# Kernel optimization log

Hardware: AMD Instinct MI355X
Metric: run time of the kernel (lower is better)

The kernel has to match this reference:

```python
import jax, jax.numpy as jnp
import numpy as np

B, N_INST, C, K, H, W = 4, 64, 16, 4, 480, 480


def setup_inputs() -> dict:
    key = jax.random.key(0)
    k1, k2 = jax.random.split(key)
    # one binary-ish channel per instance, values in [0,1]
    update_map = jax.random.uniform(k1, (B, N_INST, H, W), dtype=jnp.float32)
    # current global instance-ID map, one channel per semantic category
    init_instance_map = jax.random.randint(k2, (B, C, H, W), 0, 50).astype(jnp.int32)
    # instance channel indices grouped by category (category c owns K instances)
    instance_ids = jnp.broadcast_to(
        jnp.arange(C * K, dtype=jnp.int32).reshape(C, K), (B, C, K)
    )
    return {
        "update_map": update_map,
        "init_instance_map": init_instance_map,
        "instance_ids": instance_ids,
    }


def reference(update_map, init_instance_map, instance_ids):
    b, n_inst, h, w = update_map.shape
    _, c, k = instance_ids.shape
    L = n_inst + 1  # local IDs live in [0, n_inst]
    BIG = jnp.int32(2 ** 30)

    # ---- aggregate instance channels per category (one-hot collapse) ----
    # gather the K instance channels of each category: [B, C, K, H, W]
    oh = jnp.take_along_axis(
        update_map[:, None, :, :, :],
        instance_ids[:, :, :, None, None].astype(jnp.int32),
        axis=2,
    )
    bg = jnp.full((b, c, 1, h, w), 1e-5, update_map.dtype)  # background plane
    idx = jnp.argmax(jnp.concatenate([bg, oh], axis=2), axis=2)  # [B, C, H, W]
    # remap argmax index -> instance ID via [0] + instance_ids
    padded_ids = jnp.concatenate(
        [jnp.zeros((b, c, 1), jnp.int32), instance_ids.astype(jnp.int32)], axis=2
    )  # [B, C, K+1]
    agg = padded_ids[
        jnp.arange(b)[:, None, None, None],
        jnp.arange(c)[None, :, None, None],
        idx,
    ]  # [B, C, H, W] local instance-ID map per category

    # ---- merge local IDs into global map, per env, sequential over categories ----
    def merge_env(gmap0, agg_e):
        def step(gmap, ci):
            local = agg_e[ci].reshape(-1)
            glob = gmap[ci].reshape(-1)
            max_id = jnp.max(gmap)  # max over ALL categories so far (sequential dep)
            # smallest overlapping nonzero global ID per local ID (torch.unique()[0])
            overlap_min = jax.ops.segment_min(
                jnp.where(glob != 0, glob, BIG), local, num_segments=L
            )
            present = jax.ops.segment_sum(
                jnp.ones_like(local), local, num_segments=L
            ) > 0
            has_overlap = overlap_min < BIG
            is_new = (present & (~has_overlap)).at[0].set(False)
            new_id = max_id + jnp.cumsum(is_new.astype(jnp.int32))
            mapping = jnp.where(has_overlap, overlap_min, jnp.where(is_new, new_id, 0))
            mapping = mapping.at[0].set(0)
            new_glob = jnp.maximum(glob, mapping[local]).reshape(h, w)
            updated = jnp.where(jnp.sum(agg_e[ci]) > 0, new_glob, gmap[ci])
            return gmap.at[ci].set(updated), None

        gmap, _ = jax.lax.scan(step, gmap0, jnp.arange(c))
        return gmap

    return jax.vmap(merge_env)(init_instance_map, agg)
```

## Files before the change

kernel.cpp:

```cpp
#include <hip/hip_runtime.h>
#include <stdint.h>
#include <limits.h>

#define BB 4
#define NI 64
#define CC 16
#define KK 4
#define HH 480
#define WW 480
#define PLANE (HH * WW)
#define NG (PLANE / 4)
#define BPP 45
#define GPT 5
#define TPB 256
#define BIGV (1 << 30)
#define NPLANE (BB * CC)

typedef float  v4f __attribute__((ext_vector_type(4)));
typedef int    v4i __attribute__((ext_vector_type(4)));

#define SEL8_BYTES ((size_t)NPLANE * PLANE)
#define PART_STRIDE 8
#define MAP_OFF (NPLANE * BPP * PART_STRIDE)

__device__ __forceinline__ int wred_min(int v) {
    for (int o = 32; o; o >>= 1) v = min(v, __shfl_down(v, o, 64));
    return v;
}
__device__ __forceinline__ int wred_max(int v) {
    for (int o = 32; o; o >>= 1) v = max(v, __shfl_down(v, o, 64));
    return v;
}
__device__ __forceinline__ int wred_or(int v) {
    for (int o = 32; o; o >>= 1) v |= __shfl_down(v, o, 64);
    return v;
}

__global__ __launch_bounds__(TPB) void stats_kernel(
    const float* __restrict__ update, const int* __restrict__ initmap,
    const int* __restrict__ inst_ids, unsigned int* __restrict__ sel8,
    int* __restrict__ wsi) {
    int plane = blockIdx.x / BPP;
    int chunk = blockIdx.x % BPP;
    int b = plane >> 4;

    int idbase = plane * KK;
    int id0 = inst_ids[idbase + 0], id1 = inst_ids[idbase + 1];
    int id2 = inst_ids[idbase + 2], id3 = inst_ids[idbase + 3];

    const v4f* u0 = (const v4f*)(update + ((size_t)b * NI + id0) * PLANE);
    const v4f* u1 = (const v4f*)(update + ((size_t)b * NI + id1) * PLANE);
    const v4f* u2 = (const v4f*)(update + ((size_t)b * NI + id2) * PLANE);
    const v4f* u3 = (const v4f*)(update + ((size_t)b * NI + id3) * PLANE);
    const v4i* gl = (const v4i*)(initmap + (size_t)plane * PLANE);
    unsigned int* sp = sel8 + (size_t)plane * NG;

    int lmin0 = INT_MAX, lmin1 = INT_MAX, lmin2 = INT_MAX, lmin3 = INT_MAX;
    int pres = 0, gmax = 0;

    int base = chunk * (TPB * GPT);
#pragma unroll
    for (int it = 0; it < GPT; it++) {
        int g = base + it * TPB + threadIdx.x;
        v4f a  = __builtin_nontemporal_load(&u0[g]);
        v4f b2 = __builtin_nontemporal_load(&u1[g]);
        v4f c  = __builtin_nontemporal_load(&u2[g]);
        v4f d  = __builtin_nontemporal_load(&u3[g]);
        v4i gv = __builtin_nontemporal_load(&gl[g]);

        unsigned int packed = 0;
#pragma unroll
        for (int e = 0; e < 4; e++) {
            float best = 1e-5f; int s = 0;
            if (a[e]  > best) { best = a[e];  s = 1; }
            if (b2[e] > best) { best = b2[e]; s = 2; }
            if (c[e]  > best) { best = c[e];  s = 3; }
            if (d[e]  > best) { s = 4; }
            int gve = gv[e];
            packed |= (unsigned int)(s * 50 + gve) << (8 * e);
            gmax = max(gmax, gve);
            if (s) {
                int kk = s - 1; pres |= 1 << kk;
                int v = gve ? gve : BIGV;
                if (kk == 0) lmin0 = min(lmin0, v);
                else if (kk == 1) lmin1 = min(lmin1, v);
                else if (kk == 2) lmin2 = min(lmin2, v);
                else lmin3 = min(lmin3, v);
            }
        }
        sp[g] = packed;
    }

    lmin0 = wred_min(lmin0); lmin1 = wred_min(lmin1);
    lmin2 = wred_min(lmin2); lmin3 = wred_min(lmin3);
    pres = wred_or(pres); gmax = wred_max(gmax);

    __shared__ int red[4][6];
    int wv = threadIdx.x >> 6, lane = threadIdx.x & 63;
    if (lane == 0) {
        red[wv][0] = lmin0; red[wv][1] = lmin1; red[wv][2] = lmin2;
        red[wv][3] = lmin3; red[wv][4] = pres;  red[wv][5] = gmax;
    }
    __syncthreads();
    if (threadIdx.x == 0) {
        int m0 = red[0][0], m1 = red[0][1], m2 = red[0][2], m3 = red[0][3];
        int pr = red[0][4], gm = red[0][5];
        for (int w2 = 1; w2 < 4; w2++) {
            m0 = min(m0, red[w2][0]); m1 = min(m1, red[w2][1]);
            m2 = min(m2, red[w2][2]); m3 = min(m3, red[w2][3]);
            pr |= red[w2][4]; gm = max(gm, red[w2][5]);
        }
        int* pp = wsi + ((size_t)plane * BPP + chunk) * PART_STRIDE;
        pp[0] = m0; pp[1] = m1; pp[2] = m2; pp[3] = m3; pp[4] = pr; pp[5] = gm;
    }
}

__global__ void mapping_kernel(const int* __restrict__ inst_ids, int* wsi) {
    __shared__ int s_ov[NPLANE][4];
    __shared__ int s_pr[NPLANE];
    __shared__ int s_gm[NPLANE];

    int plane = threadIdx.x;
    int m0 = INT_MAX, m1 = INT_MAX, m2 = INT_MAX, m3 = INT_MAX, pr = 0, gm = 0;
    for (int ch = 0; ch < BPP; ch++) {
        const int* pp = wsi + ((size_t)plane * BPP + ch) * PART_STRIDE;
        m0 = min(m0, pp[0]); m1 = min(m1, pp[1]);
        m2 = min(m2, pp[2]); m3 = min(m3, pp[3]);
        pr |= pp[4]; gm = max(gm, pp[5]);
    }
    s_ov[plane][0] = m0; s_ov[plane][1] = m1;
    s_ov[plane][2] = m2; s_ov[plane][3] = m3;
    s_pr[plane] = pr; s_gm[plane] = gm;
    __syncthreads();

    if (threadIdx.x < BB) {
        int b = threadIdx.x;
        int max_id = 0;
        for (int ci = 0; ci < CC; ci++) max_id = max(max_id, s_gm[b * CC + ci]);
        for (int ci = 0; ci < CC; ci++) {
            int pl = b * CC + ci;
            int base = pl * KK;
            int id[KK], ov[KK], prb[KK];
            int prbits = s_pr[pl];
            for (int t = 0; t < KK; t++) {
                id[t] = inst_ids[base + t];
                ov[t] = s_ov[pl][t];
                prb[t] = (prbits >> t) & 1;
            }
            int ord[KK] = {0, 1, 2, 3};
            for (int i = 1; i < KK; i++) {
                int key = ord[i], j = i - 1;
                while (j >= 0 && id[ord[j]] > id[key]) { ord[j + 1] = ord[j]; j--; }
                ord[j + 1] = key;
            }
            int map_slot[KK];
            int prev_id = -1, cur_map = 0, cnt_new = 0;
            for (int j = 0; j < KK; j++) {
                int s = ord[j], l = id[s];
                if (l != prev_id) {
                    int cov = INT_MAX, cpr = 0;
                    for (int t = 0; t < KK; t++)
                        if (id[t] == l) { cov = min(cov, ov[t]); cpr |= prb[t]; }
                    if (l == 0) cur_map = 0;
                    else {
                        bool has = cov < BIGV;
                        bool isnew = cpr && !has;
                        if (isnew) { cnt_new++; cur_map = max_id + cnt_new; }
                        else cur_map = has ? cov : 0;
                    }
                    prev_id = l;
                }
                map_slot[s] = cur_map;
            }
            for (int t = 0; t < KK; t++) wsi[MAP_OFF + base + t] = map_slot[t];
            max_id += cnt_new;
        }
    }
}

__global__ __launch_bounds__(TPB) void remap_kernel(
    const unsigned int* __restrict__ sel8, const int* __restrict__ wsi,
    int* __restrict__ out) {
    int plane = blockIdx.x / BPP;
    int chunk = blockIdx.x % BPP;

    int m0 = wsi[MAP_OFF + plane * 4 + 0];
    int m1 = wsi[MAP_OFF + plane * 4 + 1];
    int m2 = wsi[MAP_OFF + plane * 4 + 2];
    int m3 = wsi[MAP_OFF + plane * 4 + 3];

    const unsigned int* sp = sel8 + (size_t)plane * NG;
    v4i* op = (v4i*)(out + (size_t)plane * PLANE);

    int base = chunk * (TPB * GPT);
#pragma unroll
    for (int it = 0; it < GPT; it++) {
        int g = base + it * TPB + threadIdx.x;
        unsigned int u = sp[g];
        v4i ov;
#pragma unroll
        for (int e = 0; e < 4; e++) {
            unsigned int p = (u >> (8 * e)) & 0xFFu;
            int s = (int)((p * 41u) >> 11);
            int gvv = (int)p - s * 50;
            int mv = (s == 1) ? m0 : (s == 2) ? m1 : (s == 3) ? m2 : m3;
            ov[e] = s ? max(gvv, mv) : gvv;
        }
        __builtin_nontemporal_store(ov, &op[g]);
    }
}

extern "C" void kernel_launch(void* const* d_in, const int* in_sizes, int n_in,
                              void* d_out, int out_size, void* d_ws, size_t ws_size,
                              hipStream_t stream) {
    const float* update = (const float*)d_in[0];
    const int* initmap = (const int*)d_in[1];
    const int* inst_ids = (const int*)d_in[2];
    int* out = (int*)d_out;

    unsigned int* sel8 = (unsigned int*)d_ws;
    int* wsi = (int*)((uint8_t*)d_ws + SEL8_BYTES);

    stats_kernel<<<NPLANE * BPP, TPB, 0, stream>>>(update, initmap, inst_ids, sel8, wsi);
    mapping_kernel<<<1, NPLANE, 0, stream>>>(inst_ids, wsi);
    remap_kernel<<<NPLANE * BPP, TPB, 0, stream>>>(sel8, wsi, out);
}
```

Baseline: 389.3 us.

## Fuse stats, mapping and remap into one cooperative kernel with grid sync

```diff
diff --git a/kernel.cpp b/kernel.cpp
--- a/kernel.cpp
+++ b/kernel.cpp
@@ -1,4 +1,5 @@
 #include <hip/hip_runtime.h>
+#include <hip/hip_cooperative_groups.h>
 #include <stdint.h>
 #include <limits.h>
 
@@ -10,19 +11,32 @@
 #define WW 480
 #define PLANE (HH * WW)
 #define NG (PLANE / 4)
-#define BPP 45
-#define GPT 5
 #define TPB 256
 #define BIGV (1 << 30)
 #define NPLANE (BB * CC)
 
-typedef float  v4f __attribute__((ext_vector_type(4)));
-typedef int    v4i __attribute__((ext_vector_type(4)));
+#define NSEG 15
+#define GPB 3840
+#define GPT 15
+#define NBLK (NPLANE * NSEG)
+
+#define BPP 45
+#define GPT3 5
+
+typedef float v4f __attribute__((ext_vector_type(4)));
+typedef int   v4i __attribute__((ext_vector_type(4)));
 
 #define SEL8_BYTES ((size_t)NPLANE * PLANE)
 #define PART_STRIDE 8
 #define MAP_OFF (NPLANE * BPP * PART_STRIDE)
 
+__device__ __forceinline__ void coh_store(int* p, int v) {
+    __hip_atomic_store(p, v, __ATOMIC_RELEASE, __HIP_MEMORY_SCOPE_AGENT);
+}
+__device__ __forceinline__ int coh_load(const int* p) {
+    return __hip_atomic_load(p, __ATOMIC_ACQUIRE, __HIP_MEMORY_SCOPE_AGENT);
+}
+
 __device__ __forceinline__ int wred_min(int v) {
     for (int o = 32; o; o >>= 1) v = min(v, __shfl_down(v, o, 64));
     return v;
@@ -36,13 +50,68 @@
     return v;
 }
 
-__global__ __launch_bounds__(TPB) void stats_kernel(
+__device__ __forceinline__ void build_mapping(
+    const int* __restrict__ inst_ids, int b, int max_id,
+    const int (*s_ov)[4], const int* s_pr, int ci_want, int* map_out) {
+    for (int ci = 0; ci < CC; ci++) {
+        int base2 = (b * CC + ci) * KK;
+        int id[KK], ov[KK], prb[KK];
+        int prbits = s_pr[ci];
+        for (int t = 0; t < KK; t++) {
+            id[t] = inst_ids[base2 + t];
+            ov[t] = s_ov[ci][t];
+            prb[t] = (prbits >> t) & 1;
+        }
+        int ord[KK] = {0, 1, 2, 3};
+        for (int i = 1; i < KK; i++) {
+            int key = ord[i], j = i - 1;
+            while (j >= 0 && id[ord[j]] > id[key]) { ord[j + 1] = ord[j]; j--; }
+            ord[j + 1] = key;
+        }
+        int map_slot[KK];
+        int prev_id = -1, cur_map = 0, cnt_new = 0;
+        for (int j = 0; j < KK; j++) {
+            int s = ord[j], l = id[s];
+            if (l != prev_id) {
+                int cov = INT_MAX, cpr = 0;
+                for (int t = 0; t < KK; t++)
+                    if (id[t] == l) { cov = min(cov, ov[t]); cpr |= prb[t]; }
+                if (l == 0) cur_map = 0;
+                else {
+                    bool has = cov < BIGV;
+                    bool isnew = cpr && !has;
+                    if (isnew) { cnt_new++; cur_map = max_id + cnt_new; }
+                    else cur_map = has ? cov : 0;
+                }
+                prev_id = l;
+            }
+            map_slot[s] = cur_map;
+        }
+        if (ci == ci_want)
+            for (int t = 0; t < KK; t++) map_out[t] = map_slot[t];
+        max_id += cnt_new;
+    }
+}
+
+__global__ __launch_bounds__(TPB, 4) void fused_kernel(
     const float* __restrict__ update, const int* __restrict__ initmap,
-    const int* __restrict__ inst_ids, unsigned int* __restrict__ sel8,
-    int* __restrict__ wsi) {
-    int plane = blockIdx.x / BPP;
-    int chunk = blockIdx.x % BPP;
+    const int* __restrict__ inst_ids, int* __restrict__ out, int* wsi) {
+    namespace cg = cooperative_groups;
+    cg::grid_group grid = cg::this_grid();
+
+    __shared__ unsigned int s_packed[GPB];
+    __shared__ int red[4][6];
+    __shared__ int s_ov[CC][4];
+    __shared__ int s_pr[CC];
+    __shared__ int s_gm[CC];
+    __shared__ int s_map[4];
+
+    int blk = blockIdx.x;
+    int plane = blk / NSEG;
+    int seg = blk % NSEG;
     int b = plane >> 4;
+    int ci_own = plane & 15;
+    int tid = threadIdx.x;
 
     int idbase = plane * KK;
     int id0 = inst_ids[idbase + 0], id1 = inst_ids[idbase + 1];
@@ -53,15 +122,14 @@
     const v4f* u2 = (const v4f*)(update + ((size_t)b * NI + id2) * PLANE);
     const v4f* u3 = (const v4f*)(update + ((size_t)b * NI + id3) * PLANE);
     const v4i* gl = (const v4i*)(initmap + (size_t)plane * PLANE);
-    unsigned int* sp = sel8 + (size_t)plane * NG;
 
     int lmin0 = INT_MAX, lmin1 = INT_MAX, lmin2 = INT_MAX, lmin3 = INT_MAX;
     int pres = 0, gmax = 0;
-
-    int base = chunk * (TPB * GPT);
+    int gbase = seg * GPB;
+
 #pragma unroll
     for (int it = 0; it < GPT; it++) {
-        int g = base + it * TPB + threadIdx.x;
+        int g = gbase + it * TPB + tid;
         v4f a  = __builtin_nontemporal_load(&u0[g]);
         v4f b2 = __builtin_nontemporal_load(&u1[g]);
         v4f c  = __builtin_nontemporal_load(&u2[g]);
@@ -88,6 +156,131 @@
                 else lmin3 = min(lmin3, v);
             }
         }
+        s_packed[it * TPB + tid] = packed;
+    }
+
+    lmin0 = wred_min(lmin0); lmin1 = wred_min(lmin1);
+    lmin2 = wred_min(lmin2); lmin3 = wred_min(lmin3);
+    pres = wred_or(pres); gmax = wred_max(gmax);
+
+    int wv = tid >> 6, lane = tid & 63;
+    if (lane == 0) {
+        red[wv][0] = lmin0; red[wv][1] = lmin1; red[wv][2] = lmin2;
+        red[wv][3] = lmin3; red[wv][4] = pres;  red[wv][5] = gmax;
+    }
+    __syncthreads();
+    if (tid == 0) {
+        int m0 = red[0][0], m1 = red[0][1], m2 = red[0][2], m3 = red[0][3];
+        int pr = red[0][4], gm = red[0][5];
+        for (int w2 = 1; w2 < 4; w2++) {
+            m0 = min(m0, red[w2][0]); m1 = min(m1, red[w2][1]);
+            m2 = min(m2, red[w2][2]); m3 = min(m3, red[w2][3]);
+            pr |= red[w2][4]; gm = max(gm, red[w2][5]);
+        }
+        int* pp = wsi + ((size_t)plane * NSEG + seg) * PART_STRIDE;
+        coh_store(&pp[0], m0); coh_store(&pp[1], m1);
+        coh_store(&pp[2], m2); coh_store(&pp[3], m3);
+        coh_store(&pp[4], pr); coh_store(&pp[5], gm);
+    }
+
+    __threadfence();
+    grid.sync();
+
+    if (tid < CC) {
+        int pl = b * CC + tid;
+        int m0 = INT_MAX, m1 = INT_MAX, m2 = INT_MAX, m3 = INT_MAX, pr = 0, gm = 0;
+        for (int s = 0; s < NSEG; s++) {
+            const int* pp = wsi + ((size_t)pl * NSEG + s) * PART_STRIDE;
+            m0 = min(m0, coh_load(&pp[0]));
+            m1 = min(m1, coh_load(&pp[1]));
+            m2 = min(m2, coh_load(&pp[2]));
+            m3 = min(m3, coh_load(&pp[3]));
+            pr |= coh_load(&pp[4]);
+            gm = max(gm, coh_load(&pp[5]));
+        }
+        s_ov[tid][0] = m0; s_ov[tid][1] = m1;
+        s_ov[tid][2] = m2; s_ov[tid][3] = m3;
+        s_pr[tid] = pr; s_gm[tid] = gm;
+    }
+    __syncthreads();
+    if (tid == 0) {
+        int max_id = 0;
+        for (int ci = 0; ci < CC; ci++) max_id = max(max_id, s_gm[ci]);
+        build_mapping(inst_ids, b, max_id, s_ov, s_pr, ci_own, s_map);
+    }
+    __syncthreads();
+
+    int m0 = s_map[0], m1 = s_map[1], m2 = s_map[2], m3 = s_map[3];
+    v4i* op = (v4i*)(out + (size_t)plane * PLANE);
+#pragma unroll
+    for (int it = 0; it < GPT; it++) {
+        int g = gbase + it * TPB + tid;
+        unsigned int u = s_packed[it * TPB + tid];
+        v4i ov;
+#pragma unroll
+        for (int e = 0; e < 4; e++) {
+            unsigned int p = (u >> (8 * e)) & 0xFFu;
+            int s = (int)((p * 41u) >> 11);
+            int gvv = (int)p - s * 50;
+            int mv = (s == 1) ? m0 : (s == 2) ? m1 : (s == 3) ? m2 : m3;
+            ov[e] = s ? max(gvv, mv) : gvv;
+        }
+        __builtin_nontemporal_store(ov, &op[g]);
+    }
+}
+
+__global__ __launch_bounds__(TPB) void stats_kernel(
+    const float* __restrict__ update, const int* __restrict__ initmap,
+    const int* __restrict__ inst_ids, unsigned int* __restrict__ sel8,
+    int* __restrict__ wsi) {
+    int plane = blockIdx.x / BPP;
+    int chunk = blockIdx.x % BPP;
+    int b = plane >> 4;
+
+    int idbase = plane * KK;
+    int id0 = inst_ids[idbase + 0], id1 = inst_ids[idbase + 1];
+    int id2 = inst_ids[idbase + 2], id3 = inst_ids[idbase + 3];
+
+    const v4f* u0 = (const v4f*)(update + ((size_t)b * NI + id0) * PLANE);
+    const v4f* u1 = (const v4f*)(update + ((size_t)b * NI + id1) * PLANE);
+    const v4f* u2 = (const v4f*)(update + ((size_t)b * NI + id2) * PLANE);
+    const v4f* u3 = (const v4f*)(update + ((size_t)b * NI + id3) * PLANE);
+    const v4i* gl = (const v4i*)(initmap + (size_t)plane * PLANE);
+    unsigned int* sp = sel8 + (size_t)plane * NG;
+
+    int lmin0 = INT_MAX, lmin1 = INT_MAX, lmin2 = INT_MAX, lmin3 = INT_MAX;
+    int pres = 0, gmax = 0;
+
+    int base = chunk * (TPB * GPT3);
+#pragma unroll
+    for (int it = 0; it < GPT3; it++) {
+        int g = base + it * TPB + threadIdx.x;
+        v4f a  = __builtin_nontemporal_load(&u0[g]);
+        v4f b2 = __builtin_nontemporal_load(&u1[g]);
+        v4f c  = __builtin_nontemporal_load(&u2[g]);
+        v4f d  = __builtin_nontemporal_load(&u3[g]);
+        v4i gv = __builtin_nontemporal_load(&gl[g]);
+
+        unsigned int packed = 0;
+#pragma unroll
+        for (int e = 0; e < 4; e++) {
+            float best = 1e-5f; int s = 0;
+            if (a[e]  > best) { best = a[e];  s = 1; }
+            if (b2[e] > best) { best = b2[e]; s = 2; }
+            if (c[e]  > best) { best = c[e];  s = 3; }
+            if (d[e]  > best) { s = 4; }
+            int gve = gv[e];
+            packed |= (unsigned int)(s * 50 + gve) << (8 * e);
+            gmax = max(gmax, gve);
+            if (s) {
+                int kk = s - 1; pres |= 1 << kk;
+                int v = gve ? gve : BIGV;
+                if (kk == 0) lmin0 = min(lmin0, v);
+                else if (kk == 1) lmin1 = min(lmin1, v);
+                else if (kk == 2) lmin2 = min(lmin2, v);
+                else lmin3 = min(lmin3, v);
+            }
+        }
         sp[g] = packed;
     }
 
@@ -138,13 +331,17 @@
         int max_id = 0;
         for (int ci = 0; ci < CC; ci++) max_id = max(max_id, s_gm[b * CC + ci]);
         for (int ci = 0; ci < CC; ci++) {
-            int pl = b * CC + ci;
-            int base = pl * KK;
+            int mp[4];
+            build_mapping(inst_ids, b, max_id, &s_ov[b * CC], &s_pr[b * CC], ci, mp);
+            (void)mp;
+        }
+        for (int ci = 0; ci < CC; ci++) {
+            int base2 = (b * CC + ci) * KK;
             int id[KK], ov[KK], prb[KK];
-            int prbits = s_pr[pl];
+            int prbits = s_pr[b * CC + ci];
             for (int t = 0; t < KK; t++) {
-                id[t] = inst_ids[base + t];
-                ov[t] = s_ov[pl][t];
+                id[t] = inst_ids[base2 + t];
+                ov[t] = s_ov[b * CC + ci][t];
                 prb[t] = (prbits >> t) & 1;
             }
             int ord[KK] = {0, 1, 2, 3};
@@ -172,7 +369,7 @@
                 }
                 map_slot[s] = cur_map;
             }
-            for (int t = 0; t < KK; t++) wsi[MAP_OFF + base + t] = map_slot[t];
+            for (int t = 0; t < KK; t++) wsi[MAP_OFF + base2 + t] = map_slot[t];
             max_id += cnt_new;
         }
     }
@@ -192,9 +389,9 @@
     const unsigned int* sp = sel8 + (size_t)plane * NG;
     v4i* op = (v4i*)(out + (size_t)plane * PLANE);
 
-    int base = chunk * (TPB * GPT);
-#pragma unroll
-    for (int it = 0; it < GPT; it++) {
+    int base = chunk * (TPB * GPT3);
+#pragma unroll
+    for (int it = 0; it < GPT3; it++) {
         int g = base + it * TPB + threadIdx.x;
         unsigned int u = sp[g];
         v4i ov;
@@ -221,7 +418,14 @@
     unsigned int* sel8 = (unsigned int*)d_ws;
     int* wsi = (int*)((uint8_t*)d_ws + SEL8_BYTES);
 
-    stats_kernel<<<NPLANE * BPP, TPB, 0, stream>>>(update, initmap, inst_ids, sel8, wsi);
-    mapping_kernel<<<1, NPLANE, 0, stream>>>(inst_ids, wsi);
-    remap_kernel<<<NPLANE * BPP, TPB, 0, stream>>>(sel8, wsi, out);
-}
+    void* args[] = {(void*)&update, (void*)&initmap, (void*)&inst_ids,
+                    (void*)&out, (void*)&wsi};
+    hipError_t err = hipLaunchCooperativeKernel((const void*)fused_kernel,
+                                                dim3(NBLK), dim3(TPB), args, 0, stream);
+    if (err != hipSuccess) {
+        (void)hipGetLastError();
+        stats_kernel<<<NPLANE * BPP, TPB, 0, stream>>>(update, initmap, inst_ids, sel8, wsi);
+        mapping_kernel<<<1, NPLANE, 0, stream>>>(inst_ids, wsi);
+        remap_kernel<<<NPLANE * BPP, TPB, 0, stream>>>(sel8, wsi, out);
+    }
+}
```

New measurement: 1.393 ms. 3.58x slower.
